# Kernel tuning notes

Hardware: AMD Instinct MI355X
Metric: run time of the kernel (lower is better)

## Reference

```python
import jax, jax.numpy as jnp
import numpy as np

# Crossbar constants (from iterator / hard-coded in source)
V_REF = 0.25
G_MIN = 0.001
G_MAX = 0.005
N_AVG = 2.8
N_STD = 0.2

N_IN, N_OUT, BATCH = 1024, 512, 128


def setup_inputs() -> dict:
    key = jax.random.key(0)
    ks = jax.random.split(key, 6)
    stdv = 1.0 / np.sqrt(N_IN)
    x = jax.random.normal(ks[0], (BATCH, N_IN), jnp.float32)
    w_pos = 0.5 + stdv * jax.random.normal(ks[1], (N_IN, N_OUT), jnp.float32)
    w_neg = 0.5 + stdv * jax.random.normal(ks[2], (N_IN, N_OUT), jnp.float32)
    b_pos = jnp.full((N_OUT,), 0.5, jnp.float32)
    b_neg = jnp.full((N_OUT,), 0.5, jnp.float32)
    # per-device nonlinearity noise for the (n_in+1, 2*n_out) crossbar
    n_noise = jax.random.normal(ks[3], (N_IN + 1, 2 * N_OUT), jnp.float32)
    return {"x": x, "w_pos": w_pos, "w_neg": w_neg, "b_pos": b_pos,
            "b_neg": b_neg, "n_noise": n_noise}


def reference(x, w_pos, w_neg, b_pos, b_neg, n_noise):
    # --- assemble combined weights: biases appended as extra word line,
    # pos/neg columns interleaved -> (m, 2*n_out), m = n_in+1
    cw_pos = jnp.concatenate([w_pos, b_pos[None, :]], axis=0)
    cw_neg = jnp.concatenate([w_neg, b_neg[None, :]], axis=0)
    m = cw_pos.shape[0]
    weights = jnp.stack([cw_pos, cw_neg], axis=-1).reshape(m, -1)  # (m, 2*n_out)

    # --- map weight params to conductances: G = k_G * w + G_min
    max_weight = jnp.max(jnp.abs(weights))
    k_G = (G_MAX - G_MIN) / max_weight
    G = k_G * weights + G_MIN                      # (m, 2*n_out)

    # --- map inputs to voltages (extra column of ones for bias line)
    k_V = 2.0 * V_REF
    ones = jnp.ones((x.shape[0], 1), x.dtype)
    V = k_V * jnp.concatenate([x, ones], axis=1)   # (b, m)

    # --- nonlinear device currents: I = sign(V) * V_ref*G * (|V|/V_ref)^log2(n)
    n = N_AVG + N_STD * n_noise                    # (m, 2*n_out)
    exponent = jnp.log2(n)
    ratio = jnp.abs(V) / V_REF                     # (b, m)
    I_ind = (jnp.sign(V)[:, :, None]
             * (V_REF * G)[None, :, :]
             * ratio[:, :, None] ** exponent[None, :, :])  # (b, m, 2*n_out)

    # --- bit-line reduction, pos-neg differential, map current back to y
    I = jnp.sum(I_ind, axis=1)                     # (b, 2*n_out)
    I_total = I[:, 0::2] - I[:, 1::2]              # (b, n_out)
    y = I_total / (k_V * k_G)
    return y
```

## Files before the change

### kernel.cpp

```cpp
#include <hip/hip_runtime.h>

#define N_IN  1024
#define N_OUT 512
#define BATCH 128
#define M     (N_IN + 1)

#define WS_MAXP_OFF 0
#define WS_LS_OFF   1024
#define WS_LS_BYTES ((size_t)M * BATCH * 8)
#define WS_NEEDED   (WS_LS_OFF + WS_LS_BYTES)

#if defined(__has_builtin)
#  if __has_builtin(__builtin_amdgcn_exp2f)
#    define FAST_EXP2(x) __builtin_amdgcn_exp2f(x)
#  endif
#  if __has_builtin(__builtin_amdgcn_logf)
#    define FAST_LOG2(x) __builtin_amdgcn_logf(x)
#  endif
#endif
#ifndef FAST_EXP2
#  define FAST_EXP2(x) exp2f(x)
#endif
#ifndef FAST_LOG2
#  define FAST_LOG2(x) log2f(x)
#endif

#define MAXRED_BLOCKS 256
#define PREP_BLOCKS   ((M * BATCH + 255) / 256)

__global__ __launch_bounds__(256)
void setup_kernel(const float4* __restrict__ wp4, const float4* __restrict__ wn4,
                  const float* __restrict__ bp, const float* __restrict__ bn,
                  const float* __restrict__ x,
                  float* __restrict__ maxp, float2* __restrict__ LS)
{
    const int bid = blockIdx.x;
    if (bid < MAXRED_BLOCKS) {
        const int t = threadIdx.x;
        const int base = bid * 512;
        float m = 0.0f;
        #pragma unroll
        for (int r = 0; r < 2; ++r) {
            const float4 a = wp4[base + r * 256 + t];
            const float4 b = wn4[base + r * 256 + t];
            m = fmaxf(m, fmaxf(fmaxf(fabsf(a.x), fabsf(a.y)),
                               fmaxf(fabsf(a.z), fabsf(a.w))));
            m = fmaxf(m, fmaxf(fmaxf(fabsf(b.x), fabsf(b.y)),
                               fmaxf(fabsf(b.z), fabsf(b.w))));
        }
        if (bid == 0) {
            m = fmaxf(m, fmaxf(fabsf(bp[t]), fabsf(bp[t + 256])));
            m = fmaxf(m, fmaxf(fabsf(bn[t]), fabsf(bn[t + 256])));
        }
        #pragma unroll
        for (int off = 32; off > 0; off >>= 1)
            m = fmaxf(m, __shfl_xor(m, off, 64));
        __shared__ float wred[4];
        const int wid = threadIdx.x >> 6;
        if ((threadIdx.x & 63) == 0) wred[wid] = m;
        __syncthreads();
        if (threadIdx.x == 0)
            maxp[bid] = fmaxf(fmaxf(wred[0], wred[1]), fmaxf(wred[2], wred[3]));
    } else {
        const int idx = (bid - MAXRED_BLOCKS) * 256 + threadIdx.x;
        if (idx >= M * BATCH) return;
        const int i = idx >> 7;
        const int b = idx & 127;
        float l = 1.0f, s = 1.0f;
        if (i < N_IN) {
            const float v = x[b * N_IN + i];
            s = (v > 0.0f) ? 1.0f : ((v < 0.0f) ? -1.0f : 0.0f);
            l = FAST_LOG2(2.0f * fabsf(v));
        }
        LS[idx] = make_float2(l, s);
    }
}

#define IC  61
#define CH2 17

__global__ __launch_bounds__(256)
void memristor_main(const float* __restrict__ wp, const float* __restrict__ wn,
                    const float* __restrict__ bp, const float* __restrict__ bn,
                    const float* __restrict__ nn, const float* __restrict__ maxp,
                    const float2* __restrict__ LS, float* __restrict__ y)
{
    const int jlane = threadIdx.x & 63;
    const int bslot = __builtin_amdgcn_readfirstlane((int)(threadIdx.x >> 6));

    float m = fmaxf(fmaxf(maxp[jlane], maxp[jlane + 64]),
                    fmaxf(maxp[jlane + 128], maxp[jlane + 192]));
    #pragma unroll
    for (int off = 32; off > 0; off >>= 1)
        m = fmaxf(m, __shfl_xor(m, off, 64));
    const float gofs = 0.125f * __uint_as_float(
        __builtin_amdgcn_readfirstlane(__float_as_uint(m)));

    int bid = blockIdx.x;
    const int jt = bid & 7;
    const int bt = (bid >> 3) & 3;
    const int ic = bid >> 5;

    const int i0   = ic * CH2;
    const int iend = (i0 + CH2 < M) ? (i0 + CH2) : M;
    const int j    = jt * 64 + jlane;
    const int b0   = bt * 32 + bslot * 8;

    float acc[8];
    #pragma unroll
    for (int k = 0; k < 8; ++k) acc[k] = 0.0f;

    for (int i = i0; i < iend; ++i) {
        float wpv, wnv;
        if (i < N_IN) {
            wpv = wp[i * N_OUT + j];
            wnv = wn[i * N_OUT + j];
        } else {
            wpv = bp[j];
            wnv = bn[j];
        }
        const float2 np2 = reinterpret_cast<const float2*>(nn)[i * N_OUT + j];
        const float ep = FAST_LOG2(fmaf(0.2f, np2.x, 2.8f));
        const float en = FAST_LOG2(fmaf(0.2f, np2.y, 2.8f));
        const float gp = fmaf(0.5f, wpv, gofs);
        const float gn = fmaf(0.5f, wnv, gofs);
        const int lsb = i * BATCH + b0;
        #pragma unroll
        for (int k = 0; k < 8; ++k) {
            const float2 p = LS[lsb + k];
            const float Ep = FAST_EXP2(ep * p.x);
            const float En = FAST_EXP2(en * p.x);
            acc[k] = fmaf(p.y, fmaf(gp, Ep, -(gn * En)), acc[k]);
        }
    }

    #pragma unroll
    for (int k = 0; k < 8; ++k)
        atomicAdd(&y[(b0 + k) * N_OUT + j], acc[k]);
}

extern "C" void kernel_launch(void* const* d_in, const int* in_sizes, int n_in,
                              void* d_out, int out_size, void* d_ws, size_t ws_size,
                              hipStream_t stream)
{
    const float* x  = (const float*)d_in[0];
    const float* wp = (const float*)d_in[1];
    const float* wn = (const float*)d_in[2];
    const float* bp = (const float*)d_in[3];
    const float* bn = (const float*)d_in[4];
    const float* nn = (const float*)d_in[5];
    float* y        = (float*)d_out;

    float*  maxp = (float*)((char*)d_ws + WS_MAXP_OFF);
    float2* LS   = (float2*)((char*)d_ws + WS_LS_OFF);

    (void)hipMemsetAsync(y, 0, (size_t)out_size * sizeof(float), stream);

    setup_kernel<<<MAXRED_BLOCKS + PREP_BLOCKS, 256, 0, stream>>>(
        (const float4*)wp, (const float4*)wn, bp, bn, x, maxp, LS);

    memristor_main<<<8 * 4 * IC, 256, 0, stream>>>(wp, wn, bp, bn, nn,
                                                   maxp, LS, y);
}
```

Measured before the change: 99.11 us.

## Fuse input log/sign prep into main kernel via shared memory, drop memset

```diff
diff --git a/kernel.cpp b/kernel.cpp
--- a/kernel.cpp
+++ b/kernel.cpp
@@ -5,10 +5,6 @@
 #define BATCH 128
 #define M     (N_IN + 1)
 
-#define WS_MAXP_OFF 0
-#define WS_LS_OFF   1024
-#define WS_LS_BYTES ((size_t)M * BATCH * 8)
-#define WS_NEEDED   (WS_LS_OFF + WS_LS_BYTES)
 
 #if defined(__has_builtin)
 #  if __has_builtin(__builtin_amdgcn_exp2f)
@@ -25,68 +21,78 @@
 #  define FAST_LOG2(x) log2f(x)
 #endif
 
-#define MAXRED_BLOCKS 256
-#define PREP_BLOCKS   ((M * BATCH + 255) / 256)
+__global__ __launch_bounds__(256)
+void maxred_kernel(const float4* __restrict__ wp4, const float4* __restrict__ wn4,
+                   const float* __restrict__ bp, const float* __restrict__ bn,
+                   float* __restrict__ maxp, float* __restrict__ y)
+{
+    const int bid = blockIdx.x;
+    const int t   = threadIdx.x;
+
+    y[bid * 256 + t] = 0.0f;
+
+    const int base = bid * 512;
+    float m = 0.0f;
+    #pragma unroll
+    for (int r = 0; r < 2; ++r) {
+        const float4 a = wp4[base + r * 256 + t];
+        const float4 b = wn4[base + r * 256 + t];
+        m = fmaxf(m, fmaxf(fmaxf(fabsf(a.x), fabsf(a.y)),
+                           fmaxf(fabsf(a.z), fabsf(a.w))));
+        m = fmaxf(m, fmaxf(fmaxf(fabsf(b.x), fabsf(b.y)),
+                           fmaxf(fabsf(b.z), fabsf(b.w))));
+    }
+    if (bid == 0) {
+        m = fmaxf(m, fmaxf(fabsf(bp[t]), fabsf(bp[t + 256])));
+        m = fmaxf(m, fmaxf(fabsf(bn[t]), fabsf(bn[t + 256])));
+    }
+    #pragma unroll
+    for (int off = 32; off > 0; off >>= 1)
+        m = fmaxf(m, __shfl_xor(m, off, 64));
+
+    __shared__ float wred[4];
+    const int wid = t >> 6;
+    if ((t & 63) == 0) wred[wid] = m;
+    __syncthreads();
+    if (t == 0)
+        maxp[bid] = fmaxf(fmaxf(wred[0], wred[1]), fmaxf(wred[2], wred[3]));
+}
+
+#define CH 16
+#define IC 64
 
 __global__ __launch_bounds__(256)
-void setup_kernel(const float4* __restrict__ wp4, const float4* __restrict__ wn4,
-                  const float* __restrict__ bp, const float* __restrict__ bn,
-                  const float* __restrict__ x,
-                  float* __restrict__ maxp, float2* __restrict__ LS)
+void memristor_main(const float* __restrict__ x,  const float* __restrict__ wp,
+                    const float* __restrict__ wn, const float* __restrict__ bp,
+                    const float* __restrict__ bn, const float* __restrict__ nn,
+                    const float* __restrict__ maxp, float* __restrict__ y)
 {
+    __shared__ float2 lsbuf[32][CH];
+
+    const int jlane = threadIdx.x & 63;
+    const int bslot = __builtin_amdgcn_readfirstlane((int)(threadIdx.x >> 6));
+
     const int bid = blockIdx.x;
-    if (bid < MAXRED_BLOCKS) {
-        const int t = threadIdx.x;
-        const int base = bid * 512;
-        float m = 0.0f;
+    const int jt  = bid & 7;
+    const int bt  = (bid >> 3) & 3;
+    const int ic  = bid >> 5;
+
+    const int i0 = ic * CH;
+    const int j  = jt * 64 + jlane;
+    const int b0 = bt * 32;
+
+    {
+        const int ii = threadIdx.x & 15;
+        const int bb = threadIdx.x >> 4;
         #pragma unroll
         for (int r = 0; r < 2; ++r) {
-            const float4 a = wp4[base + r * 256 + t];
-            const float4 b = wn4[base + r * 256 + t];
-            m = fmaxf(m, fmaxf(fmaxf(fabsf(a.x), fabsf(a.y)),
-                               fmaxf(fabsf(a.z), fabsf(a.w))));
-            m = fmaxf(m, fmaxf(fmaxf(fabsf(b.x), fabsf(b.y)),
-                               fmaxf(fabsf(b.z), fabsf(b.w))));
+            const int bbb = bb + r * 16;
+            const float v = x[(b0 + bbb) * N_IN + i0 + ii];
+            const float s = (v > 0.0f) ? 1.0f : ((v < 0.0f) ? -1.0f : 0.0f);
+            const float l = FAST_LOG2(2.0f * fabsf(v));
+            lsbuf[bbb][ii] = make_float2(l, s);
         }
-        if (bid == 0) {
-            m = fmaxf(m, fmaxf(fabsf(bp[t]), fabsf(bp[t + 256])));
-            m = fmaxf(m, fmaxf(fabsf(bn[t]), fabsf(bn[t + 256])));
-        }
-        #pragma unroll
-        for (int off = 32; off > 0; off >>= 1)
-            m = fmaxf(m, __shfl_xor(m, off, 64));
-        __shared__ float wred[4];
-        const int wid = threadIdx.x >> 6;
-        if ((threadIdx.x & 63) == 0) wred[wid] = m;
-        __syncthreads();
-        if (threadIdx.x == 0)
-            maxp[bid] = fmaxf(fmaxf(wred[0], wred[1]), fmaxf(wred[2], wred[3]));
-    } else {
-        const int idx = (bid - MAXRED_BLOCKS) * 256 + threadIdx.x;
-        if (idx >= M * BATCH) return;
-        const int i = idx >> 7;
-        const int b = idx & 127;
-        float l = 1.0f, s = 1.0f;
-        if (i < N_IN) {
-            const float v = x[b * N_IN + i];
-            s = (v > 0.0f) ? 1.0f : ((v < 0.0f) ? -1.0f : 0.0f);
-            l = FAST_LOG2(2.0f * fabsf(v));
-        }
-        LS[idx] = make_float2(l, s);
     }
-}
-
-#define IC  61
-#define CH2 17
-
-__global__ __launch_bounds__(256)
-void memristor_main(const float* __restrict__ wp, const float* __restrict__ wn,
-                    const float* __restrict__ bp, const float* __restrict__ bn,
-                    const float* __restrict__ nn, const float* __restrict__ maxp,
-                    const float2* __restrict__ LS, float* __restrict__ y)
-{
-    const int jlane = threadIdx.x & 63;
-    const int bslot = __builtin_amdgcn_readfirstlane((int)(threadIdx.x >> 6));
 
     float m = fmaxf(fmaxf(maxp[jlane], maxp[jlane + 64]),
                     fmaxf(maxp[jlane + 128], maxp[jlane + 192]));
@@ -96,47 +102,48 @@
     const float gofs = 0.125f * __uint_as_float(
         __builtin_amdgcn_readfirstlane(__float_as_uint(m)));
 
-    int bid = blockIdx.x;
-    const int jt = bid & 7;
-    const int bt = (bid >> 3) & 3;
-    const int ic = bid >> 5;
-
-    const int i0   = ic * CH2;
-    const int iend = (i0 + CH2 < M) ? (i0 + CH2) : M;
-    const int j    = jt * 64 + jlane;
-    const int b0   = bt * 32 + bslot * 8;
+    __syncthreads();
 
     float acc[8];
     #pragma unroll
     for (int k = 0; k < 8; ++k) acc[k] = 0.0f;
 
-    for (int i = i0; i < iend; ++i) {
-        float wpv, wnv;
-        if (i < N_IN) {
-            wpv = wp[i * N_OUT + j];
-            wnv = wn[i * N_OUT + j];
-        } else {
-            wpv = bp[j];
-            wnv = bn[j];
-        }
-        const float2 np2 = reinterpret_cast<const float2*>(nn)[i * N_OUT + j];
+    const float*  wprow = wp + (size_t)i0 * N_OUT + j;
+    const float*  wnrow = wn + (size_t)i0 * N_OUT + j;
+    const float2* nnrow = (const float2*)nn + (size_t)i0 * N_OUT + j;
+
+    #pragma unroll 4
+    for (int ii = 0; ii < CH; ++ii) {
+        const float wpv = wprow[ii * N_OUT];
+        const float wnv = wnrow[ii * N_OUT];
+        const float2 np2 = nnrow[ii * N_OUT];
         const float ep = FAST_LOG2(fmaf(0.2f, np2.x, 2.8f));
         const float en = FAST_LOG2(fmaf(0.2f, np2.y, 2.8f));
         const float gp = fmaf(0.5f, wpv, gofs);
         const float gn = fmaf(0.5f, wnv, gofs);
-        const int lsb = i * BATCH + b0;
         #pragma unroll
         for (int k = 0; k < 8; ++k) {
-            const float2 p = LS[lsb + k];
+            const float2 p = lsbuf[bslot * 8 + k][ii];
             const float Ep = FAST_EXP2(ep * p.x);
             const float En = FAST_EXP2(en * p.x);
             acc[k] = fmaf(p.y, fmaf(gp, Ep, -(gn * En)), acc[k]);
         }
     }
 
+    if (ic == IC - 1) {
+        const float2 np2 = ((const float2*)nn)[(size_t)N_IN * N_OUT + j];
+        const float npp = fmaf(0.2f, np2.x, 2.8f);
+        const float npn = fmaf(0.2f, np2.y, 2.8f);
+        const float gp = fmaf(0.5f, bp[j], gofs);
+        const float gn = fmaf(0.5f, bn[j], gofs);
+        const float t  = fmaf(gp, npp, -(gn * npn));
+        #pragma unroll
+        for (int k = 0; k < 8; ++k) acc[k] += t;
+    }
+
     #pragma unroll
     for (int k = 0; k < 8; ++k)
-        atomicAdd(&y[(b0 + k) * N_OUT + j], acc[k]);
+        atomicAdd(&y[(b0 + bslot * 8 + k) * N_OUT + j], acc[k]);
 }
 
 extern "C" void kernel_launch(void* const* d_in, const int* in_sizes, int n_in,
@@ -150,15 +157,11 @@
     const float* bn = (const float*)d_in[4];
     const float* nn = (const float*)d_in[5];
     float* y        = (float*)d_out;
+    float* maxp     = (float*)d_ws;
 
-    float*  maxp = (float*)((char*)d_ws + WS_MAXP_OFF);
-    float2* LS   = (float2*)((char*)d_ws + WS_LS_OFF);
+    maxred_kernel<<<256, 256, 0, stream>>>((const float4*)wp, (const float4*)wn,
+                                           bp, bn, maxp, y);
 
-    (void)hipMemsetAsync(y, 0, (size_t)out_size * sizeof(float), stream);
-
-    setup_kernel<<<MAXRED_BLOCKS + PREP_BLOCKS, 256, 0, stream>>>(
-        (const float4*)wp, (const float4*)wn, bp, bn, x, maxp, LS);
-
-    memristor_main<<<8 * 4 * IC, 256, 0, stream>>>(wp, wn, bp, bn, nn,
-                                                   maxp, LS, y);
+    memristor_main<<<8 * 4 * IC, 256, 0, stream>>>(x, wp, wn, bp, bn, nn,
+                                                   maxp, y);
 }
```

After: 91.96 us. 1.08x faster.
